# Kernel tuning notes

Measured on AMD Instinct MI355X. Metric: run time of the kernel, lower is better.

The kernel has to match this reference:

```python
import jax, jax.numpy as jnp
import numpy as np

N_SPK, N_UTT, D = 512, 64, 1024
EPS = 1e-6  # matches tf.math.l2_normalize default epsilon guard


def _l2norm(x, axis=-1):
    return x / jnp.sqrt(jnp.maximum(jnp.sum(x * x, axis=axis, keepdims=True), EPS))


def setup_inputs() -> dict:
    key = jax.random.key(0)
    k1, _ = jax.random.split(key)
    inputs = jax.random.normal(k1, (N_SPK, N_UTT, D), dtype=jnp.float32)
    w = jnp.asarray(10.0, dtype=jnp.float32)
    b = jnp.asarray(-5.0, dtype=jnp.float32)
    return {"inputs": inputs, "w": w, "b": b}


def reference(inputs, w, b):
    N, M, _ = inputs.shape
    # speaker centroids: mean over utterances -> [N, D]
    centroids = jnp.mean(inputs, axis=1)
    # utterance (exclusion) centroids: mean of the other M-1 utterances -> [N, M, D]
    ut_centroids = (jnp.sum(inputs, axis=1, keepdims=True) - inputs) / (M - 1)

    e = _l2norm(inputs)          # [N, M, D]
    c = _l2norm(centroids)       # [N, D]
    uc = _l2norm(ut_centroids)   # [N, M, D]

    # cosine sim of every utterance vs every speaker centroid -> [N, M, K]
    cos_all = jnp.einsum('nmd,kd->nmk', e, c)
    # same-speaker entries use the self-exclusion centroid
    cos_self = jnp.sum(e * uc, axis=-1)  # [N, M]
    eye = jnp.eye(N, dtype=inputs.dtype)[:, None, :]  # [N, 1, N]
    cos_sim = cos_all * (1.0 - eye) + cos_self[:, :, None] * eye

    sim = w * cos_sim + b  # [N, M, N]
    # softmax contrastive loss: -S_{j,i,j} + logsumexp_k S_{j,i,k}, summed
    lse = jax.nn.logsumexp(sim, axis=-1)            # [N, M]
    pos = jnp.einsum('nmn->nm', sim)                # diagonal along speaker axes
    loss = jnp.sum(lse - pos)
    return loss
```

## Files before the change

kernel.cpp:

```cpp
#include <hip/hip_runtime.h>
#include <stdint.h>

#define N_SPK 512
#define N_UTT 64
#define DIM   1024
#define NROWS (N_SPK * N_UTT)
#define EPS   1e-6f

#define BM 128
#define BN 128
#define BK 32
#define KTILES (DIM / BK)

typedef __attribute__((ext_vector_type(8))) short short8;
typedef __attribute__((ext_vector_type(4))) float f32x4;

__device__ __forceinline__ uint16_t f2bf(float f) {
    union { float f; uint32_t i; } un; un.f = f;
    uint32_t x = un.i;
    return (uint16_t)((x + 0x7fffu + ((x >> 16) & 1u)) >> 16);
}

__global__ __launch_bounds__(256) void prep_stream(
    const float* __restrict__ x, uint16_t* __restrict__ xb,
    float* __restrict__ Sg, float* __restrict__ xxg)
{
    const int b    = blockIdx.x;
    const int n    = b >> 2;
    const int g    = b & 3;
    const int tid  = threadIdx.x;
    const int lane = tid & 63;
    const int w    = tid >> 6;

    const float* xn  = x  + (size_t)n * N_UTT * DIM;
    uint16_t*    xbn = xb + (size_t)n * N_UTT * DIM;

    float Sp[16];
    #pragma unroll
    for (int j = 0; j < 16; ++j) Sp[j] = 0.f;

    #pragma unroll
    for (int i = 0; i < 4; ++i) {
        const int m = g * 16 + w * 4 + i;
        const float* rp = xn  + (size_t)m * DIM;
        uint16_t*    op = xbn + (size_t)m * DIM;
        float xxp = 0.f;
        #pragma unroll
        for (int j = 0; j < 4; ++j) {
            const float4 v = *(const float4*)(rp + j * 256 + lane * 4);
            xxp += v.x * v.x + v.y * v.y + v.z * v.z + v.w * v.w;
            Sp[j * 4 + 0] += v.x; Sp[j * 4 + 1] += v.y;
            Sp[j * 4 + 2] += v.z; Sp[j * 4 + 3] += v.w;
            ushort4 o;
            o.x = f2bf(v.x); o.y = f2bf(v.y); o.z = f2bf(v.z); o.w = f2bf(v.w);
            *(ushort4*)(op + j * 256 + lane * 4) = o;
        }
        #pragma unroll
        for (int off = 1; off < 64; off <<= 1) xxp += __shfl_xor(xxp, off);
        if (lane == 0) xxg[n * N_UTT + m] = xxp;
    }

    __shared__ float Sh[4][DIM];
    #pragma unroll
    for (int j = 0; j < 4; ++j)
        *(float4*)&Sh[w][j * 256 + lane * 4] =
            make_float4(Sp[j * 4], Sp[j * 4 + 1], Sp[j * 4 + 2], Sp[j * 4 + 3]);
    __syncthreads();

    const int d0 = tid * 4;
    float4 a = *(const float4*)&Sh[0][d0];
    const float4 b1 = *(const float4*)&Sh[1][d0];
    const float4 b2 = *(const float4*)&Sh[2][d0];
    const float4 b3 = *(const float4*)&Sh[3][d0];
    a.x += b1.x + b2.x + b3.x; a.y += b1.y + b2.y + b3.y;
    a.z += b1.z + b2.z + b3.z; a.w += b1.w + b2.w + b3.w;
    float* Sgn = Sg + (size_t)n * DIM + d0;
    atomicAdd(Sgn + 0, a.x); atomicAdd(Sgn + 1, a.y);
    atomicAdd(Sgn + 2, a.z); atomicAdd(Sgn + 3, a.w);
}

__global__ __launch_bounds__(256) void centroid_kernel(
    const float* __restrict__ Sg, uint16_t* __restrict__ cmat, float* __restrict__ ssqg)
{
    const int n   = blockIdx.x;
    const int tid = threadIdx.x;
    const int d0  = tid * 4;

    const float4 S = *(const float4*)(Sg + (size_t)n * DIM + d0);
    float css = S.x * S.x + S.y * S.y + S.z * S.z + S.w * S.w;
    #pragma unroll
    for (int off = 1; off < 64; off <<= 1) css += __shfl_xor(css, off);
    __shared__ float red[4];
    if ((tid & 63) == 0) red[tid >> 6] = css;
    __syncthreads();
    const float ssq = red[0] + red[1] + red[2] + red[3];

    const float scale = rsqrtf(fmaxf(ssq * (1.0f / 4096.f), EPS)) * (1.0f / 64.f);
    ushort4 o;
    o.x = f2bf(S.x * scale); o.y = f2bf(S.y * scale);
    o.z = f2bf(S.z * scale); o.w = f2bf(S.w * scale);
    *(ushort4*)(cmat + (size_t)n * DIM + d0) = o;
    if (tid == 0) ssqg[n] = ssq;
}

__global__ __launch_bounds__(256) void gemm_lse_kernel(
    const uint16_t* __restrict__ xb, const uint16_t* __restrict__ cmat,
    const float* __restrict__ xxg, const float* __restrict__ ssqg,
    const float* __restrict__ wp, const float* __restrict__ bp,
    float* __restrict__ sumexp, float* __restrict__ pos)
{
    __shared__ uint16_t Asm[BM * BK];
    __shared__ uint16_t Bsm[BN * BK];

    const int tid   = threadIdx.x;
    const int lane  = tid & 63;
    const int wid   = tid >> 6;
    const int waveM = wid >> 1;
    const int waveN = wid & 1;

    const int bid = blockIdx.x;
    const int rt  = (bid & 7) | ((bid >> 5) << 3);
    const int ct  = (bid >> 3) & 3;

    const int rowBase = rt * BM;
    const int colBase = ct * BN;

    const uint16_t* gA[2];
    const uint16_t* gB[2];
    #pragma unroll
    for (int i = 0; i < 2; ++i) {
        const int s    = i * 256 + tid;
        const int srow = s >> 2;
        const int kc   = (s & 3) ^ ((srow >> 1) & 3);
        gA[i] = xb   + (size_t)(rowBase + srow) * DIM + kc * 8;
        gB[i] = cmat + (size_t)(colBase + srow) * DIM + kc * 8;
    }

    f32x4 acc[4][4];
    #pragma unroll
    for (int i = 0; i < 4; ++i)
        #pragma unroll
        for (int j = 0; j < 4; ++j)
            acc[i][j] = (f32x4){0.f, 0.f, 0.f, 0.f};

    const int cL  = lane & 15;
    const int q   = lane >> 4;
    const int key = (cL >> 1) & 3;
    const int kcs = q ^ key;

    for (int kt = 0; kt < KTILES; ++kt) {
        __syncthreads();
        const int ko = kt * BK;
        #pragma unroll
        for (int i = 0; i < 2; ++i) {
            __builtin_amdgcn_global_load_lds(
                (const __attribute__((address_space(1))) void*)(gA[i] + ko),
                (__attribute__((address_space(3))) void*)(&Asm[(i * 256 + wid * 64) * 8]),
                16, 0, 0);
            __builtin_amdgcn_global_load_lds(
                (const __attribute__((address_space(1))) void*)(gB[i] + ko),
                (__attribute__((address_space(3))) void*)(&Bsm[(i * 256 + wid * 64) * 8]),
                16, 0, 0);
        }
        __syncthreads();

        short8 a[4], b[4];
        #pragma unroll
        for (int bi = 0; bi < 4; ++bi)
            a[bi] = *(const short8*)&Asm[(waveM * 64 + bi * 16 + cL) * BK + kcs * 8];
        #pragma unroll
        for (int bj = 0; bj < 4; ++bj)
            b[bj] = *(const short8*)&Bsm[(waveN * 64 + bj * 16 + cL) * BK + kcs * 8];

        #pragma unroll
        for (int bi = 0; bi < 4; ++bi)
            #pragma unroll
            for (int bj = 0; bj < 4; ++bj)
                acc[bi][bj] = __builtin_amdgcn_mfma_f32_16x16x32_bf16(
                    a[bi], b[bj], acc[bi][bj], 0, 0, 0);
    }

    const float wv = wp[0], bv = bp[0];
    #pragma unroll
    for (int bi = 0; bi < 4; ++bi) {
        #pragma unroll
        for (int r = 0; r < 4; ++r) {
            const int R    = rowBase + waveM * 64 + bi * 16 + q * 4 + r;
            const float xxv = xxg[R];
            const float rn  = rsqrtf(fmaxf(xxv, EPS));
            const int nrow  = R >> 6;
            float s = 0.f;
            #pragma unroll
            for (int bj = 0; bj < 4; ++bj) {
                const int col = colBase + waveN * 64 + bj * 16 + cL;
                const float dot = acc[bi][bj][r];
                float sim;
                if (col == nrow) {
                    const float ssqv = ssqg[nrow];
                    const float xs   = dot * sqrtf(ssqv);
                    const float d2   = ssqv - 2.f * xs + xxv;
                    const float cs   = ((xs - xxv) * (1.f / 63.f)) * rn *
                                       rsqrtf(fmaxf(d2 * (1.f / 3969.f), EPS));
                    sim = wv * cs + bv;
                    pos[R] = sim;
                } else {
                    sim = wv * (dot * rn) + bv;
                }
                s += __expf(sim);
            }
            #pragma unroll
            for (int off = 1; off < 16; off <<= 1) s += __shfl_xor(s, off);
            if (cL == 0) atomicAdd(&sumexp[R], s);
        }
    }
}

__global__ __launch_bounds__(256) void finalize_kernel(
    const float* __restrict__ pos, const float* __restrict__ sumexp,
    float* __restrict__ out)
{
    const int tid = blockIdx.x * 256 + threadIdx.x;
    float acc = 0.f;
    for (int r = tid; r < NROWS; r += 64 * 256)
        acc += __logf(sumexp[r]) - pos[r];
    #pragma unroll
    for (int off = 1; off < 64; off <<= 1) acc += __shfl_xor(acc, off);
    __shared__ float red[4];
    if ((threadIdx.x & 63) == 0) red[threadIdx.x >> 6] = acc;
    __syncthreads();
    if (threadIdx.x == 0)
        atomicAdd(out, red[0] + red[1] + red[2] + red[3]);
}

extern "C" void kernel_launch(void* const* d_in, const int* in_sizes, int n_in,
                              void* d_out, int out_size, void* d_ws, size_t ws_size,
                              hipStream_t stream)
{
    const float* x  = (const float*)d_in[0];
    const float* wp = (const float*)d_in[1];
    const float* bp = (const float*)d_in[2];
    float* out = (float*)d_out;

    char* ws = (char*)d_ws;
    size_t off = 0;
    uint16_t* xb     = (uint16_t*)(ws + off); off += (size_t)NROWS * DIM * 2;
    uint16_t* cmat   = (uint16_t*)(ws + off); off += (size_t)N_SPK * DIM * 2;
    float*    Sg     = (float*)(ws + off);    off += (size_t)N_SPK * DIM * 4;
    float*    xxg    = (float*)(ws + off);    off += (size_t)NROWS * 4;
    float*    pos    = (float*)(ws + off);    off += (size_t)NROWS * 4;
    float*    sumexp = (float*)(ws + off);    off += (size_t)NROWS * 4;
    float*    ssqg   = (float*)(ws + off);    off += (size_t)N_SPK * 4;

    hipMemsetAsync(Sg, 0, (size_t)N_SPK * DIM * sizeof(float), stream);
    hipMemsetAsync(sumexp, 0, NROWS * sizeof(float), stream);
    hipMemsetAsync(out, 0, sizeof(float), stream);

    prep_stream<<<N_SPK * 4, 256, 0, stream>>>(x, xb, Sg, xxg);
    centroid_kernel<<<N_SPK, 256, 0, stream>>>(Sg, cmat, ssqg);
    gemm_lse_kernel<<<(NROWS / BM) * (N_SPK / BN), 256, 0, stream>>>(
        xb, cmat, xxg, ssqg, wp, bp, sumexp, pos);
    finalize_kernel<<<64, 256, 0, stream>>>(pos, sumexp, out);
}
```

Before: 284.3 us.

## Replace atomics and memsets with partial-sum buffers reduced downstream

```diff
diff --git a/kernel.cpp b/kernel.cpp
--- a/kernel.cpp
+++ b/kernel.cpp
@@ -23,7 +23,7 @@
 
 __global__ __launch_bounds__(256) void prep_stream(
     const float* __restrict__ x, uint16_t* __restrict__ xb,
-    float* __restrict__ Sg, float* __restrict__ xxg)
+    float* __restrict__ Sg4, float* __restrict__ xxg)
 {
     const int b    = blockIdx.x;
     const int n    = b >> 2;
@@ -34,30 +34,40 @@
 
     const float* xn  = x  + (size_t)n * N_UTT * DIM;
     uint16_t*    xbn = xb + (size_t)n * N_UTT * DIM;
+    const int m0 = g * 16 + w * 4;
+
+    float4 v[16];
+    #pragma unroll
+    for (int i = 0; i < 4; ++i)
+        #pragma unroll
+        for (int j = 0; j < 4; ++j)
+            v[i * 4 + j] = *(const float4*)(xn + (size_t)(m0 + i) * DIM + j * 256 + lane * 4);
 
     float Sp[16];
     #pragma unroll
     for (int j = 0; j < 16; ++j) Sp[j] = 0.f;
+    float xx[4] = {0.f, 0.f, 0.f, 0.f};
 
     #pragma unroll
     for (int i = 0; i < 4; ++i) {
-        const int m = g * 16 + w * 4 + i;
-        const float* rp = xn  + (size_t)m * DIM;
-        uint16_t*    op = xbn + (size_t)m * DIM;
-        float xxp = 0.f;
         #pragma unroll
         for (int j = 0; j < 4; ++j) {
-            const float4 v = *(const float4*)(rp + j * 256 + lane * 4);
-            xxp += v.x * v.x + v.y * v.y + v.z * v.z + v.w * v.w;
-            Sp[j * 4 + 0] += v.x; Sp[j * 4 + 1] += v.y;
-            Sp[j * 4 + 2] += v.z; Sp[j * 4 + 3] += v.w;
+            const float4 q = v[i * 4 + j];
+            xx[i] += q.x * q.x + q.y * q.y + q.z * q.z + q.w * q.w;
+            Sp[j * 4 + 0] += q.x; Sp[j * 4 + 1] += q.y;
+            Sp[j * 4 + 2] += q.z; Sp[j * 4 + 3] += q.w;
             ushort4 o;
-            o.x = f2bf(v.x); o.y = f2bf(v.y); o.z = f2bf(v.z); o.w = f2bf(v.w);
-            *(ushort4*)(op + j * 256 + lane * 4) = o;
+            o.x = f2bf(q.x); o.y = f2bf(q.y); o.z = f2bf(q.z); o.w = f2bf(q.w);
+            *(ushort4*)(xbn + (size_t)(m0 + i) * DIM + j * 256 + lane * 4) = o;
         }
-        #pragma unroll
-        for (int off = 1; off < 64; off <<= 1) xxp += __shfl_xor(xxp, off);
-        if (lane == 0) xxg[n * N_UTT + m] = xxp;
+    }
+
+    #pragma unroll
+    for (int i = 0; i < 4; ++i) {
+        float t = xx[i];
+        #pragma unroll
+        for (int off = 1; off < 64; off <<= 1) t += __shfl_xor(t, off);
+        if (lane == 0) xxg[n * N_UTT + m0 + i] = t;
     }
 
     __shared__ float Sh[4][DIM];
@@ -74,19 +84,23 @@
     const float4 b3 = *(const float4*)&Sh[3][d0];
     a.x += b1.x + b2.x + b3.x; a.y += b1.y + b2.y + b3.y;
     a.z += b1.z + b2.z + b3.z; a.w += b1.w + b2.w + b3.w;
-    float* Sgn = Sg + (size_t)n * DIM + d0;
-    atomicAdd(Sgn + 0, a.x); atomicAdd(Sgn + 1, a.y);
-    atomicAdd(Sgn + 2, a.z); atomicAdd(Sgn + 3, a.w);
+    *(float4*)(Sg4 + ((size_t)g * N_SPK + n) * DIM + d0) = a;
 }
 
 __global__ __launch_bounds__(256) void centroid_kernel(
-    const float* __restrict__ Sg, uint16_t* __restrict__ cmat, float* __restrict__ ssqg)
+    const float* __restrict__ Sg4, uint16_t* __restrict__ cmat, float* __restrict__ ssqg)
 {
     const int n   = blockIdx.x;
     const int tid = threadIdx.x;
     const int d0  = tid * 4;
 
-    const float4 S = *(const float4*)(Sg + (size_t)n * DIM + d0);
+    float4 S = *(const float4*)(Sg4 + ((size_t)0 * N_SPK + n) * DIM + d0);
+    #pragma unroll
+    for (int g = 1; g < 4; ++g) {
+        const float4 p = *(const float4*)(Sg4 + ((size_t)g * N_SPK + n) * DIM + d0);
+        S.x += p.x; S.y += p.y; S.z += p.z; S.w += p.w;
+    }
+
     float css = S.x * S.x + S.y * S.y + S.z * S.z + S.w * S.w;
     #pragma unroll
     for (int off = 1; off < 64; off <<= 1) css += __shfl_xor(css, off);
@@ -107,10 +121,11 @@
     const uint16_t* __restrict__ xb, const uint16_t* __restrict__ cmat,
     const float* __restrict__ xxg, const float* __restrict__ ssqg,
     const float* __restrict__ wp, const float* __restrict__ bp,
-    float* __restrict__ sumexp, float* __restrict__ pos)
+    float* __restrict__ sumexp4, float* __restrict__ pos)
 {
     __shared__ uint16_t Asm[BM * BK];
     __shared__ uint16_t Bsm[BN * BK];
+    __shared__ float    SeLDS[BM];
 
     const int tid   = threadIdx.x;
     const int lane  = tid & 63;
@@ -181,11 +196,12 @@
     }
 
     const float wv = wp[0], bv = bp[0];
+    float srow[16];
     #pragma unroll
     for (int bi = 0; bi < 4; ++bi) {
         #pragma unroll
         for (int r = 0; r < 4; ++r) {
-            const int R    = rowBase + waveM * 64 + bi * 16 + q * 4 + r;
+            const int R     = rowBase + waveM * 64 + bi * 16 + q * 4 + r;
             const float xxv = xxg[R];
             const float rn  = rsqrtf(fmaxf(xxv, EPS));
             const int nrow  = R >> 6;
@@ -210,26 +226,50 @@
             }
             #pragma unroll
             for (int off = 1; off < 16; off <<= 1) s += __shfl_xor(s, off);
-            if (cL == 0) atomicAdd(&sumexp[R], s);
+            srow[bi * 4 + r] = s;
         }
     }
-}
-
-__global__ __launch_bounds__(256) void finalize_kernel(
-    const float* __restrict__ pos, const float* __restrict__ sumexp,
+
+    if (waveN == 1 && cL == 0) {
+        #pragma unroll
+        for (int bi = 0; bi < 4; ++bi)
+            #pragma unroll
+            for (int r = 0; r < 4; ++r)
+                SeLDS[waveM * 64 + bi * 16 + q * 4 + r] = srow[bi * 4 + r];
+    }
+    __syncthreads();
+    if (waveN == 0 && cL == 0) {
+        #pragma unroll
+        for (int bi = 0; bi < 4; ++bi)
+            #pragma unroll
+            for (int r = 0; r < 4; ++r) {
+                const int lr = waveM * 64 + bi * 16 + q * 4 + r;
+                sumexp4[(size_t)ct * NROWS + rowBase + lr] = srow[bi * 4 + r] + SeLDS[lr];
+            }
+    }
+}
+
+__global__ __launch_bounds__(1024) void finalize_kernel(
+    const float* __restrict__ pos, const float* __restrict__ se4,
     float* __restrict__ out)
 {
-    const int tid = blockIdx.x * 256 + threadIdx.x;
+    const int tid = threadIdx.x;
     float acc = 0.f;
-    for (int r = tid; r < NROWS; r += 64 * 256)
-        acc += __logf(sumexp[r]) - pos[r];
+    for (int r = tid; r < NROWS; r += 1024) {
+        const float s = se4[r] + se4[NROWS + r] + se4[2 * NROWS + r] + se4[3 * NROWS + r];
+        acc += __logf(s) - pos[r];
+    }
     #pragma unroll
     for (int off = 1; off < 64; off <<= 1) acc += __shfl_xor(acc, off);
-    __shared__ float red[4];
-    if ((threadIdx.x & 63) == 0) red[threadIdx.x >> 6] = acc;
-    __syncthreads();
-    if (threadIdx.x == 0)
-        atomicAdd(out, red[0] + red[1] + red[2] + red[3]);
+    __shared__ float red[16];
+    if ((tid & 63) == 0) red[tid >> 6] = acc;
+    __syncthreads();
+    if (tid == 0) {
+        float t = 0.f;
+        #pragma unroll
+        for (int i = 0; i < 16; ++i) t += red[i];
+        out[0] = t;
+    }
 }
 
 extern "C" void kernel_launch(void* const* d_in, const int* in_sizes, int n_in,
@@ -243,21 +283,17 @@
 
     char* ws = (char*)d_ws;
     size_t off = 0;
-    uint16_t* xb     = (uint16_t*)(ws + off); off += (size_t)NROWS * DIM * 2;
-    uint16_t* cmat   = (uint16_t*)(ws + off); off += (size_t)N_SPK * DIM * 2;
-    float*    Sg     = (float*)(ws + off);    off += (size_t)N_SPK * DIM * 4;
-    float*    xxg    = (float*)(ws + off);    off += (size_t)NROWS * 4;
-    float*    pos    = (float*)(ws + off);    off += (size_t)NROWS * 4;
-    float*    sumexp = (float*)(ws + off);    off += (size_t)NROWS * 4;
-    float*    ssqg   = (float*)(ws + off);    off += (size_t)N_SPK * 4;
-
-    hipMemsetAsync(Sg, 0, (size_t)N_SPK * DIM * sizeof(float), stream);
-    hipMemsetAsync(sumexp, 0, NROWS * sizeof(float), stream);
-    hipMemsetAsync(out, 0, sizeof(float), stream);
-
-    prep_stream<<<N_SPK * 4, 256, 0, stream>>>(x, xb, Sg, xxg);
-    centroid_kernel<<<N_SPK, 256, 0, stream>>>(Sg, cmat, ssqg);
+    uint16_t* xb      = (uint16_t*)(ws + off); off += (size_t)NROWS * DIM * 2;
+    uint16_t* cmat    = (uint16_t*)(ws + off); off += (size_t)N_SPK * DIM * 2;
+    float*    Sg4     = (float*)(ws + off);    off += (size_t)4 * N_SPK * DIM * 4;
+    float*    xxg     = (float*)(ws + off);    off += (size_t)NROWS * 4;
+    float*    pos     = (float*)(ws + off);    off += (size_t)NROWS * 4;
+    float*    sumexp4 = (float*)(ws + off);    off += (size_t)4 * NROWS * 4;
+    float*    ssqg    = (float*)(ws + off);    off += (size_t)N_SPK * 4;
+
+    prep_stream<<<N_SPK * 4, 256, 0, stream>>>(x, xb, Sg4, xxg);
+    centroid_kernel<<<N_SPK, 256, 0, stream>>>(Sg4, cmat, ssqg);
     gemm_lse_kernel<<<(NROWS / BM) * (N_SPK / BN), 256, 0, stream>>>(
-        xb, cmat, xxg, ssqg, wp, bp, sumexp, pos);
-    finalize_kernel<<<64, 256, 0, stream>>>(pos, sumexp, out);
-}
+        xb, cmat, xxg, ssqg, wp, bp, sumexp4, pos);
+    finalize_kernel<<<1, 1024, 0, stream>>>(pos, sumexp4, out);
+}
```

Measured after the change: 271.4 us. -4.6%, faster.
